# Performance work log

Measured on AMD Instinct MI355X. Metric: run time of the kernel, lower is better.

Reference implementation:

```python
import jax, jax.numpy as jnp
import numpy as np
from jax import lax

IMG_H, IMG_W = 800.0, 800.0
REG_WEIGHTS = (10.0, 10.0, 5.0, 5.0)
SCORE_THRESH = 0.05
NMS_THRESH = 0.5
NUM_DETECTIONS = 100
MIN_SIZE = 1.0
BBOX_XFORM_CLIP = float(np.log(1000.0 / 16.0))


def setup_inputs() -> dict:
    key = jax.random.key(0)
    k1, k2, k3, k4 = jax.random.split(key, 4)
    N, C = 1000, 81
    class_logit = jax.random.normal(k1, (N, C), dtype=jnp.float32) * 2.0
    box_regression = jax.random.normal(k2, (N, C * 4), dtype=jnp.float32)
    # proposals: valid (x1,y1,x2,y2) boxes inside the 800x800 image
    ctr = jax.random.uniform(k3, (N, 2), dtype=jnp.float32) * 800.0
    wh = jax.random.uniform(k4, (N, 2), dtype=jnp.float32) * 200.0 + 8.0
    x1y1 = jnp.clip(ctr - 0.5 * wh, 0.0, 800.0)
    x2y2 = jnp.clip(ctr + 0.5 * wh, 0.0, 800.0)
    proposal = jnp.concatenate([x1y1, x2y2], axis=1)
    return dict(class_logit=class_logit, box_regression=box_regression, proposal=proposal)


def decode_boxes(deltas, boxes):
    # deltas: [..., 4] (dx,dy,dw,dh); boxes: [..., 4] (x1,y1,x2,y2)
    wx, wy, ww, wh = REG_WEIGHTS
    widths = boxes[..., 2] - boxes[..., 0]
    heights = boxes[..., 3] - boxes[..., 1]
    ctr_x = boxes[..., 0] + 0.5 * widths
    ctr_y = boxes[..., 1] + 0.5 * heights
    dx = deltas[..., 0] / wx
    dy = deltas[..., 1] / wy
    dw = jnp.minimum(deltas[..., 2] / ww, BBOX_XFORM_CLIP)
    dh = jnp.minimum(deltas[..., 3] / wh, BBOX_XFORM_CLIP)
    pcx = dx * widths + ctr_x
    pcy = dy * heights + ctr_y
    pw = jnp.exp(dw) * widths
    ph = jnp.exp(dh) * heights
    return jnp.stack([pcx - 0.5 * pw, pcy - 0.5 * ph, pcx + 0.5 * pw, pcy + 0.5 * ph], axis=-1)


def pairwise_iou(b):
    # b: [N, 4] -> [N, N]
    area = (b[:, 2] - b[:, 0]) * (b[:, 3] - b[:, 1])
    lt = jnp.maximum(b[:, None, :2], b[None, :, :2])
    rb = jnp.minimum(b[:, None, 2:], b[None, :, 2:])
    wh = jnp.clip(rb - lt, 0.0)
    inter = wh[..., 0] * wh[..., 1]
    return inter / (area[:, None] + area[None, :] - inter + 1e-9)


def nms_one_class(boxes, scores):
    # boxes: [N, 4]; scores: [N] with invalid entries masked to -1.
    # Exact greedy NMS: sort by score desc, suppress IoU > NMS_THRESH.
    N = boxes.shape[0]
    order = jnp.argsort(-scores)
    b = boxes[order]
    s = scores[order]
    iou = pairwise_iou(b)
    valid = s > -0.5

    def body(carry, xs):
        keep, i = carry
        row, v = xs
        suppressed = jnp.any(keep & (row > NMS_THRESH))
        keep = keep.at[i].set(v & jnp.logical_not(suppressed))
        return (keep, i + 1), None

    (keep, _), _ = lax.scan(body, (jnp.zeros((N,), bool), jnp.int32(0)), (iou, valid))
    s_kept = jnp.where(keep, s, -1.0)
    top_s, top_i = lax.top_k(s_kept, NUM_DETECTIONS)  # kept are already score-sorted
    out_valid = top_s > -0.5
    out_boxes = jnp.where(out_valid[:, None], b[top_i], 0.0)
    out_scores = jnp.where(out_valid, top_s, 0.0)
    return out_boxes, out_scores, out_valid


def reference(class_logit, box_regression, proposal):
    N, C = class_logit.shape
    pred_score = jax.nn.softmax(class_logit, axis=-1)           # [N, C]
    deltas = box_regression.reshape(N, C, 4)
    boxes = decode_boxes(deltas[:, 1:, :], proposal[:, None, :])  # [N, C-1, 4]
    # clip to image (process_box)
    boxes = jnp.stack([
        jnp.clip(boxes[..., 0], 0.0, IMG_W),
        jnp.clip(boxes[..., 1], 0.0, IMG_H),
        jnp.clip(boxes[..., 2], 0.0, IMG_W),
        jnp.clip(boxes[..., 3], 0.0, IMG_H),
    ], axis=-1)
    w = boxes[..., 2] - boxes[..., 0]
    h = boxes[..., 3] - boxes[..., 1]
    score_fg = pred_score[:, 1:]                                 # [N, C-1]
    valid = (score_fg >= SCORE_THRESH) & (w >= MIN_SIZE) & (h >= MIN_SIZE)
    scores_m = jnp.where(valid, score_fg, -1.0)
    boxes_c = jnp.transpose(boxes, (1, 0, 2))                    # [C-1, N, 4]
    scores_c = scores_m.T                                        # [C-1, N]
    out_boxes, out_scores, out_valid = jax.vmap(nms_one_class)(boxes_c, scores_c)
    labels = jnp.broadcast_to(jnp.arange(1, C, dtype=jnp.int32)[:, None], out_scores.shape)
    labels = jnp.where(out_valid, labels, 0)
    # padded per-class detections: boxes [C-1, D, 4], scores/labels/valid [C-1, D]
    return out_boxes, out_scores, labels, out_valid
```

## Files before the change

kernel.cpp:

```cpp
#include <hip/hip_runtime.h>
#include <math.h>

#define N_PROP   1000
#define C_ALL    81
#define N_FG     80
#define TOPK     100
#define CAP      1024
#define IMG_WH   800.0f
#define SCORE_TH 0.05f
#define NMS_TH   0.5f
#define MIN_SZ   1.0f
#define BBOX_CLIP 4.135166556742356f

typedef unsigned long long u64;

__global__ __launch_bounds__(256) void softmax_stats_kernel(
    const float* __restrict__ logits,
    float2* __restrict__ stats)
{
    const int wave = threadIdx.x >> 6;
    const int lane = threadIdx.x & 63;
    const int n = blockIdx.x * 4 + wave;
    if (n >= N_PROP) return;
    const float* row = logits + n * C_ALL;

    float v1 = row[lane];
    float v2 = (lane < C_ALL - 64) ? row[64 + lane] : 0.f;

    float m = (lane < C_ALL - 64) ? fmaxf(v1, v2) : v1;
    #pragma unroll
    for (int off = 32; off >= 1; off >>= 1)
        m = fmaxf(m, __shfl_xor(m, off, 64));

    float s = expf(v1 - m) + ((lane < C_ALL - 64) ? expf(v2 - m) : 0.0f);
    #pragma unroll
    for (int off = 32; off >= 1; off >>= 1)
        s += __shfl_xor(s, off, 64);

    if (lane == 0) stats[n] = make_float2(m, s);
}

__global__ __launch_bounds__(256) void roihead_kernel(
    const float* __restrict__ logits,
    const float* __restrict__ boxreg,
    const float* __restrict__ prop,
    const float2* __restrict__ stats,
    float* __restrict__ out)
{
    __shared__ u64   s_key[CAP];
    __shared__ float cx1[CAP], cy1[CAP], cx2[CAP], cy2[CAP], car[CAP];
    __shared__ u64   s_skey[CAP];
    __shared__ float sx1[CAP], sy1[CAP], sx2[CAP], sy2[CAP], sar[CAP];
    __shared__ u64   s_mask[256 * 4];
    __shared__ u64   s_keep[4];
    __shared__ unsigned char s_rem[CAP];
    __shared__ int   s_cnt, s_emit;

    const int c   = blockIdx.x;
    const int tid = threadIdx.x;
    const int col = c + 1;

    const int OFF_SCORES = N_FG * TOPK * 4;
    const int OFF_LABELS = OFF_SCORES + N_FG * TOPK;
    const int OFF_VALID  = OFF_LABELS + N_FG * TOPK;

    for (int t = tid; t < TOPK * 4; t += 256) out[c * TOPK * 4 + t] = 0.0f;
    for (int t = tid; t < TOPK; t += 256) {
        out[OFF_SCORES + c * TOPK + t] = 0.0f;
        out[OFF_LABELS + c * TOPK + t] = 0.0f;
        out[OFF_VALID  + c * TOPK + t] = 0.0f;
    }
    if (tid == 0) { s_cnt = 0; s_emit = 0; }
    __syncthreads();

    for (int n = tid; n < N_PROP; n += 256) {
        float2 ms = stats[n];
        float score = expf(logits[n * C_ALL + col] - ms.x) / ms.y;

        float4 p = *(const float4*)(prop + n * 4);
        float w  = p.z - p.x;
        float h  = p.w - p.y;
        float pcx0 = p.x + 0.5f * w;
        float pcy0 = p.y + 0.5f * h;

        float4 d = *(const float4*)(boxreg + n * (C_ALL * 4) + col * 4);
        float dx = d.x / 10.0f;
        float dy = d.y / 10.0f;
        float dw = fminf(d.z / 5.0f, BBOX_CLIP);
        float dh = fminf(d.w / 5.0f, BBOX_CLIP);

        float pcx = dx * w + pcx0;
        float pcy = dy * h + pcy0;
        float pw  = expf(dw) * w;
        float ph  = expf(dh) * h;

        float x1 = fminf(fmaxf(pcx - 0.5f * pw, 0.0f), IMG_WH);
        float y1 = fminf(fmaxf(pcy - 0.5f * ph, 0.0f), IMG_WH);
        float x2 = fminf(fmaxf(pcx + 0.5f * pw, 0.0f), IMG_WH);
        float y2 = fminf(fmaxf(pcy + 0.5f * ph, 0.0f), IMG_WH);

        float bw = x2 - x1;
        float bh = y2 - y1;
        if (score >= SCORE_TH && bw >= MIN_SZ && bh >= MIN_SZ) {
            int slot = atomicAdd(&s_cnt, 1);
            unsigned int fb = __float_as_uint(score);
            s_key[slot] = ((u64)fb << 20) | ((u64)(1023 - n) << 10) | (u64)slot;
            cx1[slot] = x1; cy1[slot] = y1; cx2[slot] = x2; cy2[slot] = y2;
            car[slot] = bw * bh;
        }
    }
    __syncthreads();

    const int V = s_cnt;
    if (V == 0) return;

    for (int t = tid; t < V; t += 256) {
        u64 myk = s_key[t];
        int rank = 0;
        for (int j = 0; j < V; ++j) rank += (s_key[j] > myk) ? 1 : 0;
        s_skey[rank] = myk;
        sx1[rank] = cx1[t]; sy1[rank] = cy1[t];
        sx2[rank] = cx2[t]; sy2[rank] = cy2[t];
        sar[rank] = car[t];
    }
    __syncthreads();

    if (V <= 64) {
        if (tid < 64) {
            const int lane = tid;
            bool act = lane < V;
            float bx1 = 0.f, by1 = 0.f, bx2 = 0.f, by2 = 0.f, bar = 0.f;
            if (act) {
                bx1 = sx1[lane]; by1 = sy1[lane];
                bx2 = sx2[lane]; by2 = sy2[lane];
                bar = sar[lane];
            }
            u64 myrow = 0;
            for (int i = 0; i < V; ++i) {
                float ix1 = __shfl(bx1, i, 64);
                float iy1 = __shfl(by1, i, 64);
                float ix2 = __shfl(bx2, i, 64);
                float iy2 = __shfl(by2, i, 64);
                float iar = __shfl(bar, i, 64);
                float lx = fmaxf(ix1, bx1);
                float ly = fmaxf(iy1, by1);
                float rx = fminf(ix2, bx2);
                float ry = fminf(iy2, by2);
                float iw = fmaxf(rx - lx, 0.0f);
                float ih = fmaxf(ry - ly, 0.0f);
                float inter = iw * ih;
                float iou = inter / (iar + bar - inter + 1e-9f);
                u64 bal = __ballot(act && (iou > NMS_TH));
                if (lane == i) {
                    u64 upper = (i == 63) ? 0ull : ~((1ull << (i + 1)) - 1ull);
                    myrow = bal & upper;
                }
            }
            u64 S = 0, K = 0;
            for (int i = 0; i < V; ++i) {
                if (!((S >> i) & 1ull)) {
                    K |= 1ull << i;
                    S |= __shfl(myrow, i, 64);
                }
            }
            if (act && ((K >> lane) & 1ull)) {
                int rank = __popcll(K & ((1ull << lane) - 1ull));
                float score = __uint_as_float((unsigned int)(s_skey[lane] >> 20));
                out[(c * TOPK + rank) * 4 + 0] = bx1;
                out[(c * TOPK + rank) * 4 + 1] = by1;
                out[(c * TOPK + rank) * 4 + 2] = bx2;
                out[(c * TOPK + rank) * 4 + 3] = by2;
                out[OFF_SCORES + c * TOPK + rank] = score;
                out[OFF_LABELS + c * TOPK + rank] = (float)col;
                out[OFF_VALID  + c * TOPK + rank] = 1.0f;
            }
        }
    } else if (V <= 256) {
        const int BW = (V + 63) >> 6;
        for (int i = tid; i < V; i += 256) {
            float x1i = sx1[i], y1i = sy1[i], x2i = sx2[i], y2i = sy2[i];
            float ai  = sar[i];
            for (int w = 0; w < BW; ++w) {
                u64 mrow = 0;
                int j0 = w << 6;
                int j1 = min(V, j0 + 64);
                for (int j = max(j0, i + 1); j < j1; ++j) {
                    float lx = fmaxf(x1i, sx1[j]);
                    float ly = fmaxf(y1i, sy1[j]);
                    float rx = fminf(x2i, sx2[j]);
                    float ry = fminf(y2i, sy2[j]);
                    float iw = fmaxf(rx - lx, 0.0f);
                    float ih = fmaxf(ry - ly, 0.0f);
                    float inter = iw * ih;
                    float iou = inter / (ai + sar[j] - inter + 1e-9f);
                    if (iou > NMS_TH) mrow |= 1ull << (j - j0);
                }
                s_mask[(i << 2) + w] = mrow;
            }
        }
        __syncthreads();

        if (tid == 0) {
            u64 r0 = 0, r1 = 0, r2 = 0, r3 = 0;
            u64 k0 = 0, k1 = 0, k2 = 0, k3 = 0;
            int kept = 0;
            for (int i = 0; i < V; ++i) {
                int w = i >> 6;
                u64 bit = 1ull << (i & 63);
                u64 rw = (w == 0) ? r0 : (w == 1) ? r1 : (w == 2) ? r2 : r3;
                if (rw & bit) continue;
                if (w == 0) k0 |= bit; else if (w == 1) k1 |= bit;
                else if (w == 2) k2 |= bit; else k3 |= bit;
                if (++kept >= TOPK) break;
                const u64* mr = &s_mask[i << 2];
                r0 |= mr[0];
                if (BW > 1) r1 |= mr[1];
                if (BW > 2) r2 |= mr[2];
                if (BW > 3) r3 |= mr[3];
            }
            s_keep[0] = k0; s_keep[1] = k1; s_keep[2] = k2; s_keep[3] = k3;
        }
        __syncthreads();

        u64 kw0 = s_keep[0], kw1 = s_keep[1], kw2 = s_keep[2], kw3 = s_keep[3];
        for (int t = tid; t < V; t += 256) {
            int w = t >> 6;
            u64 kw = (w == 0) ? kw0 : (w == 1) ? kw1 : (w == 2) ? kw2 : kw3;
            if (!((kw >> (t & 63)) & 1ull)) continue;
            int rank = 0;
            if (w > 0) rank += __popcll(kw0);
            if (w > 1) rank += __popcll(kw1);
            if (w > 2) rank += __popcll(kw2);
            rank += __popcll(kw & ((1ull << (t & 63)) - 1ull));
            if (rank < TOPK) {
                float score = __uint_as_float((unsigned int)(s_skey[t] >> 20));
                out[(c * TOPK + rank) * 4 + 0] = sx1[t];
                out[(c * TOPK + rank) * 4 + 1] = sy1[t];
                out[(c * TOPK + rank) * 4 + 2] = sx2[t];
                out[(c * TOPK + rank) * 4 + 3] = sy2[t];
                out[OFF_SCORES + c * TOPK + rank] = score;
                out[OFF_LABELS + c * TOPK + rank] = (float)col;
                out[OFF_VALID  + c * TOPK + rank] = 1.0f;
            }
        }
    } else {
        for (int t = tid; t < V; t += 256) s_rem[t] = 0;
        __syncthreads();
        for (int i = 0; i < V; ++i) {
            if (s_rem[i]) continue;
            if (tid == 0) {
                int k = s_emit;
                if (k < TOPK) {
                    float score = __uint_as_float((unsigned int)(s_skey[i] >> 20));
                    out[(c * TOPK + k) * 4 + 0] = sx1[i];
                    out[(c * TOPK + k) * 4 + 1] = sy1[i];
                    out[(c * TOPK + k) * 4 + 2] = sx2[i];
                    out[(c * TOPK + k) * 4 + 3] = sy2[i];
                    out[OFF_SCORES + c * TOPK + k] = score;
                    out[OFF_LABELS + c * TOPK + k] = (float)col;
                    out[OFF_VALID  + c * TOPK + k] = 1.0f;
                }
                s_emit = k + 1;
            }
            float x1i = sx1[i], y1i = sy1[i], x2i = sx2[i], y2i = sy2[i];
            float ai  = sar[i];
            for (int jj = i + 1 + tid; jj < V; jj += 256) {
                if (s_rem[jj]) continue;
                float lx = fmaxf(x1i, sx1[jj]);
                float ly = fmaxf(y1i, sy1[jj]);
                float rx = fminf(x2i, sx2[jj]);
                float ry = fminf(y2i, sy2[jj]);
                float iw = fmaxf(rx - lx, 0.0f);
                float ih = fmaxf(ry - ly, 0.0f);
                float inter = iw * ih;
                float iou = inter / (ai + sar[jj] - inter + 1e-9f);
                if (iou > NMS_TH) s_rem[jj] = 1;
            }
            __syncthreads();
            if (s_emit >= TOPK) break;
        }
    }
}

extern "C" void kernel_launch(void* const* d_in, const int* in_sizes, int n_in,
                              void* d_out, int out_size, void* d_ws, size_t ws_size,
                              hipStream_t stream) {
    const float* class_logit = (const float*)d_in[0];
    const float* box_reg     = (const float*)d_in[1];
    const float* proposal    = (const float*)d_in[2];
    float* out = (float*)d_out;

    float2* stats = (float2*)d_ws;

    softmax_stats_kernel<<<(N_PROP + 3) / 4, 256, 0, stream>>>(class_logit, stats);
    roihead_kernel<<<N_FG, 256, 0, stream>>>(class_logit, box_reg, proposal,
                                             stats, out);
}
```

Before: 87.88 us.

## Move score filtering and box decoding into the per-proposal softmax kernel

Score computation, box decoding and filtering now run in the first kernel, which is parallel over proposals; that kernel appends survivors to per-class global candidate lists through global atomics. The per-class NMS kernel then only loads the compacted keys, sorts them, and gathers boxes by slot. This replaces the serial per-class scan over all 1000 proposals with strided boxreg loads, but adds a memset launch, global atomics and a round trip through global memory.

Result: slower. 98.62 us (+12.2%).

```diff
diff --git a/kernel.cpp b/kernel.cpp
--- a/kernel.cpp
+++ b/kernel.cpp
@@ -14,9 +14,13 @@
 
 typedef unsigned long long u64;
 
-__global__ __launch_bounds__(256) void softmax_stats_kernel(
+__global__ __launch_bounds__(256) void score_decode_kernel(
     const float* __restrict__ logits,
-    float2* __restrict__ stats)
+    const float* __restrict__ boxreg,
+    const float* __restrict__ prop,
+    int*    __restrict__ cnt,
+    u64*    __restrict__ keys,
+    float4* __restrict__ boxes)
 {
     const int wave = threadIdx.x >> 6;
     const int lane = threadIdx.x & 63;
@@ -37,24 +41,57 @@
     for (int off = 32; off >= 1; off >>= 1)
         s += __shfl_xor(s, off, 64);
 
-    if (lane == 0) stats[n] = make_float2(m, s);
+    float4 p = *(const float4*)(prop + n * 4);
+    float w  = p.z - p.x;
+    float h  = p.w - p.y;
+    float pcx0 = p.x + 0.5f * w;
+    float pcy0 = p.y + 0.5f * h;
+
+    auto emit = [&](int col, float score) {
+        if (score < SCORE_TH) return;
+        float4 d = *(const float4*)(boxreg + n * (C_ALL * 4) + col * 4);
+        float dx = d.x / 10.0f;
+        float dy = d.y / 10.0f;
+        float dw = fminf(d.z / 5.0f, BBOX_CLIP);
+        float dh = fminf(d.w / 5.0f, BBOX_CLIP);
+
+        float pcx = dx * w + pcx0;
+        float pcy = dy * h + pcy0;
+        float pw  = expf(dw) * w;
+        float ph  = expf(dh) * h;
+
+        float x1 = fminf(fmaxf(pcx - 0.5f * pw, 0.0f), IMG_WH);
+        float y1 = fminf(fmaxf(pcy - 0.5f * ph, 0.0f), IMG_WH);
+        float x2 = fminf(fmaxf(pcx + 0.5f * pw, 0.0f), IMG_WH);
+        float y2 = fminf(fmaxf(pcy + 0.5f * ph, 0.0f), IMG_WH);
+
+        if ((x2 - x1) >= MIN_SZ && (y2 - y1) >= MIN_SZ) {
+            int cls = col - 1;
+            int pos = atomicAdd(&cnt[cls], 1);
+            unsigned int fb = __float_as_uint(score);
+            keys[cls * CAP + pos] =
+                ((u64)fb << 20) | ((u64)(1023 - n) << 10) | (u64)pos;
+            boxes[cls * CAP + pos] = make_float4(x1, y1, x2, y2);
+        }
+    };
+
+    if (lane >= 1)              emit(lane,      expf(v1 - m) / s);
+    if (lane + 64 <= N_FG)      emit(lane + 64, expf(v2 - m) / s);
 }
 
-__global__ __launch_bounds__(256) void roihead_kernel(
-    const float* __restrict__ logits,
-    const float* __restrict__ boxreg,
-    const float* __restrict__ prop,
-    const float2* __restrict__ stats,
+__global__ __launch_bounds__(256) void nms_out_kernel(
+    const int*    __restrict__ cnt,
+    const u64*    __restrict__ keys,
+    const float4* __restrict__ boxes,
     float* __restrict__ out)
 {
     __shared__ u64   s_key[CAP];
-    __shared__ float cx1[CAP], cy1[CAP], cx2[CAP], cy2[CAP], car[CAP];
     __shared__ u64   s_skey[CAP];
     __shared__ float sx1[CAP], sy1[CAP], sx2[CAP], sy2[CAP], sar[CAP];
     __shared__ u64   s_mask[256 * 4];
     __shared__ u64   s_keep[4];
     __shared__ unsigned char s_rem[CAP];
-    __shared__ int   s_cnt, s_emit;
+    __shared__ int   s_emit;
 
     const int c   = blockIdx.x;
     const int tid = threadIdx.x;
@@ -70,58 +107,27 @@
         out[OFF_LABELS + c * TOPK + t] = 0.0f;
         out[OFF_VALID  + c * TOPK + t] = 0.0f;
     }
-    if (tid == 0) { s_cnt = 0; s_emit = 0; }
+    if (tid == 0) s_emit = 0;
+
+    const int V = min(cnt[c], N_PROP);
+    if (V == 0) { __syncthreads(); return; }
+
+    for (int t = tid; t < V; t += 256) s_key[t] = keys[c * CAP + t];
     __syncthreads();
-
-    for (int n = tid; n < N_PROP; n += 256) {
-        float2 ms = stats[n];
-        float score = expf(logits[n * C_ALL + col] - ms.x) / ms.y;
-
-        float4 p = *(const float4*)(prop + n * 4);
-        float w  = p.z - p.x;
-        float h  = p.w - p.y;
-        float pcx0 = p.x + 0.5f * w;
-        float pcy0 = p.y + 0.5f * h;
-
-        float4 d = *(const float4*)(boxreg + n * (C_ALL * 4) + col * 4);
-        float dx = d.x / 10.0f;
-        float dy = d.y / 10.0f;
-        float dw = fminf(d.z / 5.0f, BBOX_CLIP);
-        float dh = fminf(d.w / 5.0f, BBOX_CLIP);
-
-        float pcx = dx * w + pcx0;
-        float pcy = dy * h + pcy0;
-        float pw  = expf(dw) * w;
-        float ph  = expf(dh) * h;
-
-        float x1 = fminf(fmaxf(pcx - 0.5f * pw, 0.0f), IMG_WH);
-        float y1 = fminf(fmaxf(pcy - 0.5f * ph, 0.0f), IMG_WH);
-        float x2 = fminf(fmaxf(pcx + 0.5f * pw, 0.0f), IMG_WH);
-        float y2 = fminf(fmaxf(pcy + 0.5f * ph, 0.0f), IMG_WH);
-
-        float bw = x2 - x1;
-        float bh = y2 - y1;
-        if (score >= SCORE_TH && bw >= MIN_SZ && bh >= MIN_SZ) {
-            int slot = atomicAdd(&s_cnt, 1);
-            unsigned int fb = __float_as_uint(score);
-            s_key[slot] = ((u64)fb << 20) | ((u64)(1023 - n) << 10) | (u64)slot;
-            cx1[slot] = x1; cy1[slot] = y1; cx2[slot] = x2; cy2[slot] = y2;
-            car[slot] = bw * bh;
-        }
-    }
-    __syncthreads();
-
-    const int V = s_cnt;
-    if (V == 0) return;
 
     for (int t = tid; t < V; t += 256) {
         u64 myk = s_key[t];
         int rank = 0;
         for (int j = 0; j < V; ++j) rank += (s_key[j] > myk) ? 1 : 0;
         s_skey[rank] = myk;
-        sx1[rank] = cx1[t]; sy1[rank] = cy1[t];
-        sx2[rank] = cx2[t]; sy2[rank] = cy2[t];
-        sar[rank] = car[t];
+    }
+    __syncthreads();
+
+    for (int t = tid; t < V; t += 256) {
+        int slot = (int)(s_skey[t] & 1023u);
+        float4 b = boxes[c * CAP + slot];
+        sx1[t] = b.x; sy1[t] = b.y; sx2[t] = b.z; sy2[t] = b.w;
+        sar[t] = (b.z - b.x) * (b.w - b.y);
     }
     __syncthreads();
 
@@ -290,9 +296,13 @@
     const float* proposal    = (const float*)d_in[2];
     float* out = (float*)d_out;
 
-    float2* stats = (float2*)d_ws;
-
-    softmax_stats_kernel<<<(N_PROP + 3) / 4, 256, 0, stream>>>(class_logit, stats);
-    roihead_kernel<<<N_FG, 256, 0, stream>>>(class_logit, box_reg, proposal,
-                                             stats, out);
+    char* ws = (char*)d_ws;
+    int*    cnt   = (int*)ws;
+    u64*    keys  = (u64*)(ws + 1024);
+    float4* boxes = (float4*)(ws + 1024 + N_FG * CAP * sizeof(u64));
+
+    hipMemsetAsync(cnt, 0, N_FG * sizeof(int), stream);
+    score_decode_kernel<<<(N_PROP + 3) / 4, 256, 0, stream>>>(
+        class_logit, box_reg, proposal, cnt, keys, boxes);
+    nms_out_kernel<<<N_FG, 256, 0, stream>>>(cnt, keys, boxes, out);
 }
```
